# Kernel tuning notes

Hardware: AMD Instinct MI355X
Metric: run time of the kernel (lower is better)

The kernel has to match this reference:

```python
import jax, jax.numpy as jnp
import numpy as np

K = 3          # pred_ks
EMB_SCALE = 1.0


def _unfold(x, k):
    # torch nn.Unfold(kernel=k, padding=(k-1)//2, stride=1), channel-major (C, kh, kw)
    B, C, H, W = x.shape
    p = (k - 1) // 2
    xp = jnp.pad(x, ((0, 0), (0, 0), (p, p), (p, p)))
    pats = jnp.stack([xp[:, :, i:i + H, j:j + W] for i in range(k) for j in range(k)], axis=2)
    return pats.reshape(B, C * k * k, H, W)


def _gs2d_nearest(x, grid):
    # F.grid_sample(mode='nearest', padding_mode='zeros', align_corners=False)
    B, C, H, W = x.shape
    ix = jnp.round((grid[..., 0] + 1.0) * W / 2.0 - 0.5)
    iy = jnp.round((grid[..., 1] + 1.0) * H / 2.0 - 0.5)
    valid = (ix >= 0) & (ix <= W - 1) & (iy >= 0) & (iy <= H - 1)
    ixc = jnp.clip(ix, 0, W - 1).astype(jnp.int32)
    iyc = jnp.clip(iy, 0, H - 1).astype(jnp.int32)

    def samp(img, yy, xx, vv):
        return jnp.where(vv[None], img[:, yy, xx], 0.0)

    return jax.vmap(samp)(x, iyc, ixc, valid)


def _gs3d_trilinear(vol, coords):
    # F.grid_sample 3D, mode='bilinear', padding_mode='zeros', align_corners=False
    # vol [C,D,H,W]; coords [N,3] with (x->W, y->H, z->D)
    C, D, H, W = vol.shape
    x = (coords[:, 0] + 1.0) * W / 2.0 - 0.5
    y = (coords[:, 1] + 1.0) * H / 2.0 - 0.5
    z = (coords[:, 2] + 1.0) * D / 2.0 - 0.5
    x0, y0, z0 = jnp.floor(x), jnp.floor(y), jnp.floor(z)
    vol_f = vol.reshape(C, D * H * W)
    out = jnp.zeros((C, coords.shape[0]), vol.dtype)
    for dz in (0.0, 1.0):
        for dy in (0.0, 1.0):
            for dx in (0.0, 1.0):
                xi, yi, zi = x0 + dx, y0 + dy, z0 + dz
                wgt = (1.0 - jnp.abs(x - xi)) * (1.0 - jnp.abs(y - yi)) * (1.0 - jnp.abs(z - zi))
                valid = (xi >= 0) & (xi <= W - 1) & (yi >= 0) & (yi <= H - 1) & (zi >= 0) & (zi <= D - 1)
                idx = (jnp.clip(zi, 0, D - 1) * (H * W) + jnp.clip(yi, 0, H - 1) * W
                       + jnp.clip(xi, 0, W - 1)).astype(jnp.int32)
                out = out + vol_f[:, idx] * jnp.where(valid, wgt, 0.0)[None]
    return out


def setup_inputs() -> dict:
    key = jax.random.key(0)
    ks = jax.random.split(key, 7)
    B, H, W = 4, 64, 64
    NV, VL, NS = 16, 4, 16
    f = jnp.float32
    grid1 = jax.random.uniform(ks[0], (B, H, W, 2), f, -1.0, 1.0)
    grid2 = jax.random.uniform(ks[1], (B, H, W, 2), f, -1.0, 1.0)
    theta = jax.random.uniform(ks[2], (B,), f, -np.pi, np.pi)
    lgn = jax.random.normal(ks[3], (B, NV * VL, H, W), f)
    coefx = jax.random.uniform(ks[4], (NV, VL, VL, NS), f, -0.1, 0.1)
    coefy = jax.random.uniform(ks[5], (NV, VL, VL, NS), f, -0.1, 0.1)
    coefr = jax.random.uniform(ks[6], (NV, VL, VL, NS), f, -0.1, 0.1)
    return {"grid1": grid1, "grid2": grid2, "theta": theta, "lgn": lgn,
            "coefx": coefx, "coefy": coefy, "coefr": coefr}


def reference(grid1, grid2, theta, lgn, coefx, coefy, coefr):
    B, C, H, W = lgn.shape
    NV, VL, _, NS = coefx.shape
    KS2 = K * K
    # unfold + rearrange to [b, c*ks2, h, w]
    uf_lgn = _unfold(lgn, K)
    uf_g1 = _unfold(jnp.transpose(grid1, (0, 3, 1, 2)), K)
    # nearest-neighbor warps by grid2
    uf_lgn_t = _gs2d_nearest(uf_lgn, grid2)
    uf_g1_t = _gs2d_nearest(uf_g1, grid2)
    g1 = uf_g1_t.reshape(B, 2, KS2, H, W)
    g2 = jnp.transpose(grid2, (0, 3, 1, 2))[:, :, None]          # [b,2,1,h,w]
    d = (g2 - g1) * EMB_SCALE                                    # [b,2,ks2,h,w]
    d = jnp.transpose(d, (0, 2, 3, 4, 1)).reshape(B, KS2 * H * W, 2)
    th = jnp.broadcast_to((theta / np.pi)[:, None, None], (B, KS2 * H * W, 1))
    coords = jnp.concatenate([d, th], axis=-1).reshape(B * KS2 * H * W, 3)
    # separable coefficient volume: x along H-axis, y along D-axis, r along W-axis
    w1 = jnp.einsum('ijkn,iklm->ijlmn', coefx, coefy)            # (nv,vl,vl,D,H)
    coef = jnp.einsum('ijkmn,iklo->ijlmno', w1, coefr)           # (nv,vl,vl,D,H,W)
    vol = coef.reshape(NV * VL * VL, NS, NS, NS)
    samples = _gs3d_trilinear(vol, coords)                       # [nv*vl*vl, b*ks2*h*w]
    coef_ = samples.reshape(NV, VL, VL, B, KS2, H * W)
    coef_ = jnp.transpose(coef_, (3, 5, 4, 0, 1, 2))             # [b,hw,ks2,nv,vl,vl]
    lgn_ = uf_lgn_t.reshape(B, NV, VL, KS2, H * W)
    lgn_ = jnp.transpose(lgn_, (0, 4, 3, 1, 2))                  # [b,hw,ks2,nv,vl]
    pred = jnp.einsum('bsknij,bsknj->bsni', coef_, lgn_)         # matmul + sum over ks2
    return jnp.transpose(pred, (0, 2, 3, 1)).reshape(B, NV * VL, H, W)
```

## Files before the change

kernel.cpp:

```cpp
#include <hip/hip_runtime.h>
#include <hip/hip_fp16.h>
#include <cstdint>

#define BB   4
#define IH   64
#define IW   64
#define HWN  4096
#define NVN  16
#define NSN  16


#define EWS_OFF  (BB*HWN*64*2)
#define CWS_OFF  (EWS_OFF + BB*NVN*NSN*16*2)

struct __align__(16) H2x4 { __half2 h[4]; };
struct __align__(8)  H2x2 { __half2 a, b; };

__global__ __launch_bounds__(256) void prep_kernel(
    const float* __restrict__ lgn, const float* __restrict__ theta,
    const float* __restrict__ coefx, const float* __restrict__ coefy,
    const float* __restrict__ coefr, char* __restrict__ ws)
{
    const int blk = blockIdx.x, t = threadIdx.x;
    if (blk < 512) {
        __shared__ float tile[64][33];
        const int b      = blk >> 7;
        const int hwbase = (blk & 127) << 5;
        const float* src = lgn + (size_t)b * (64 * HWN) + hwbase;
        const int x4 = t & 7;
        const int c0 = t >> 3;
        #pragma unroll
        for (int i = 0; i < 2; ++i) {
            const int c = c0 + i * 32;
            const float4 v = *(const float4*)&src[c * HWN + x4 * 4];
            tile[c][x4 * 4 + 0] = v.x;
            tile[c][x4 * 4 + 1] = v.y;
            tile[c][x4 * 4 + 2] = v.z;
            tile[c][x4 * 4 + 3] = v.w;
        }
        __syncthreads();
        __half2* dst = (__half2*)ws + (size_t)b * (HWN * 32) + (size_t)hwbase * 32;
        const int cp = t & 31, hw0 = t >> 5;
        #pragma unroll
        for (int i = 0; i < 4; ++i) {
            const int hw = hw0 + i * 8;
            dst[hw * 32 + cp] =
                __floats2half2_rn(tile[2 * cp][hw], tile[2 * cp + 1][hw]);
        }
    } else if (blk < 544) {
        const int p  = (blk - 512) * 256 + t;
        const int b  = p >> 11, nv = (p >> 7) & 15, n = (p >> 3) & 15, q = p & 7;
        const float th  = theta[b] * 0.31830988618379067154f;
        const float zf  = (th + 1.0f) * 8.0f - 0.5f;
        const float zfl = floorf(zf);
        const float fz  = zf - zfl;
        const int   m0  = (int)zfl;
        const float wz0 = (m0 >= 0 && m0 <= 15) ? (1.0f - fz) : 0.0f;
        const float wz1 = (m0 + 1 >= 0 && m0 + 1 <= 15) ? fz : 0.0f;
        const int   m0c = min(max(m0, 0), 15), m1c = min(max(m0 + 1, 0), 15);
        float ev[2];
        #pragma unroll
        for (int s = 0; s < 2; ++s) {
            const int idx = 2 * q + s, j = idx >> 2, k2 = idx & 3;
            float e = 0.0f;
            #pragma unroll
            for (int k1 = 0; k1 < 4; ++k1) {
                const float a  = coefx[nv * 256 + (j * 4 + k1) * 16 + n];
                const float bm = wz0 * coefy[nv * 256 + (k1 * 4 + k2) * 16 + m0c]
                               + wz1 * coefy[nv * 256 + (k1 * 4 + k2) * 16 + m1c];
                e += a * bm;
            }
            ev[s] = e;
        }
        ((__half2*)(ws + EWS_OFF))[p] = __floats2half2_rn(ev[0], ev[1]);
    } else {
        const int p = (blk - 544) * 256 + t;
        if (p < 2048) {
            const int nv = p >> 7, o = (p >> 3) & 15, q = p & 7;
            const float c0 = coefr[nv * 256 + (2 * q + 0) * 16 + o];
            const float c1 = coefr[nv * 256 + (2 * q + 1) * 16 + o];
            ((__half2*)(ws + CWS_OFF))[p] = __floats2half2_rn(c0, c1);
        }
    }
}

__global__ __launch_bounds__(256) void seprot_kernel(
    const float* __restrict__ grid1,
    const float* __restrict__ grid2,
    const char*  __restrict__ ws,
    float* __restrict__ out)
{
    __shared__ H2x4 sC[16 * 49];
    __shared__ H2x4 sE[16 * 49];
    __shared__ float sOut[16][17][4];

    const int t   = threadIdx.x;
    const int blk = blockIdx.x;
    const int b      = blk >> 8;
    const int hwbase = (blk & 255) << 4;
    const int pg = t >> 4;
    const int nv = t & 15;
    const int hw = hwbase + pg;

    {
        const H2x4* Cw = (const H2x4*)(ws + CWS_OFF);
        const H2x4* Ew = (const H2x4*)(ws + EWS_OFF) + b * 512;
        #pragma unroll
        for (int k = 0; k < 2; ++k) {
            const int i   = t + k * 256;
            const int wnv = i >> 5, wo = (i >> 1) & 15, wu = i & 1;
            const int du  = wo * 49 + wnv * 3 + wu;
            sC[du] = Cw[i];
            sE[du] = Ew[i];
        }
    }
    __syncthreads();

    const float2 g2  = ((const float2*)grid2)[b * HWN + hw];
    const float  sxf = rintf((g2.x + 1.0f) * (0.5f * IW) - 0.5f);
    const float  syf = rintf((g2.y + 1.0f) * (0.5f * IH) - 0.5f);
    const bool valid = (sxf >= 0.0f) && (sxf <= (float)(IW - 1)) &&
                       (syf >= 0.0f) && (syf <= (float)(IH - 1));

    float acc[4] = {0.0f, 0.0f, 0.0f, 0.0f};

    if (valid) {
        const int sx = (int)sxf, sy = (int)syf;
        const __half2 zero2 = __floats2half2_rn(0.0f, 0.0f);

        #pragma unroll
        for (int tap = 0; tap < 9; ++tap) {
            const int di = tap / 3 - 1, dj = tap % 3 - 1;
            const int ty = sy + di, tx = sx + dj;
            const bool inb = ((unsigned)ty < (unsigned)IH) && ((unsigned)tx < (unsigned)IW);
            const int pix = min(max(ty, 0), IH - 1) * IW + min(max(tx, 0), IW - 1);

            H2x2 lgu = ((const H2x2*)ws)[(b * HWN + pix) * 16 + nv];
            __half2 lg01 = inb ? lgu.a : zero2;
            __half2 lg23 = inb ? lgu.b : zero2;

            const float2 g1 = ((const float2*)grid1)[b * HWN + pix];
            const float dxc = g2.x - g1.x;
            const float dyc = g2.y - g1.y;

            const float xf  = (dxc + 1.0f) * (0.5f * NSN) - 0.5f;
            const float xfl = floorf(xf);
            const float fx  = xf - xfl;
            const int   o0  = (int)xfl;
            const float wx0 = (o0 >= 0 && o0 <= NSN - 1) ? (1.0f - fx) : 0.0f;
            const float wx1 = (o0 + 1 >= 0 && o0 + 1 <= NSN - 1) ? fx : 0.0f;
            const int   o0c = min(max(o0, 0), NSN - 1);
            const int   o1c = min(max(o0 + 1, 0), NSN - 1);

            const float yf  = (dyc + 1.0f) * (0.5f * NSN) - 0.5f;
            const float yfl = floorf(yf);
            const float fy  = yf - yfl;
            const int   n0  = (int)yfl;
            const float wy0 = (n0 >= 0 && n0 <= NSN - 1) ? (1.0f - fy) : 0.0f;
            const float wy1 = (n0 + 1 >= 0 && n0 + 1 <= NSN - 1) ? fy : 0.0f;
            const int   n0c = min(max(n0, 0), NSN - 1);
            const int   n1c = min(max(n0 + 1, 0), NSN - 1);

            const __half2 wx0h = __floats2half2_rn(wx0, wx0);
            const __half2 wx1h = __floats2half2_rn(wx1, wx1);
            const __half2 wy0h = __floats2half2_rn(wy0, wy0);
            const __half2 wy1h = __floats2half2_rn(wy1, wy1);

            const H2x4 c0a = sC[o0c * 49 + nv * 3 + 0];
            const H2x4 c0b = sC[o0c * 49 + nv * 3 + 1];
            const H2x4 c1a = sC[o1c * 49 + nv * 3 + 0];
            const H2x4 c1b = sC[o1c * 49 + nv * 3 + 1];
            __half2 bl[8];
            #pragma unroll
            for (int k = 0; k < 4; ++k) {
                bl[k]     = __hfma2(c0a.h[k], wx0h, __hmul2(c1a.h[k], wx1h));
                bl[4 + k] = __hfma2(c0b.h[k], wx0h, __hmul2(c1b.h[k], wx1h));
            }
            float vf[4];
            #pragma unroll
            for (int k2 = 0; k2 < 4; ++k2) {
                const __half2 sv = __hfma2(bl[2 * k2 + 1], lg23,
                                           __hmul2(bl[2 * k2], lg01));
                vf[k2] = __low2float(sv) + __high2float(sv);
            }
            const __half2 v01 = __floats2half2_rn(vf[0], vf[1]);
            const __half2 v23 = __floats2half2_rn(vf[2], vf[3]);

            const H2x4 e0a = sE[n0c * 49 + nv * 3 + 0];
            const H2x4 e0b = sE[n0c * 49 + nv * 3 + 1];
            const H2x4 e1a = sE[n1c * 49 + nv * 3 + 0];
            const H2x4 e1b = sE[n1c * 49 + nv * 3 + 1];
            __half2 eb[8];
            #pragma unroll
            for (int k = 0; k < 4; ++k) {
                eb[k]     = __hfma2(e0a.h[k], wy0h, __hmul2(e1a.h[k], wy1h));
                eb[4 + k] = __hfma2(e0b.h[k], wy0h, __hmul2(e1b.h[k], wy1h));
            }
            #pragma unroll
            for (int j = 0; j < 4; ++j) {
                const __half2 sa = __hfma2(eb[2 * j + 1], v23,
                                           __hmul2(eb[2 * j], v01));
                acc[j] += __low2float(sa) + __high2float(sa);
            }
        }
    }

    *(float4*)&sOut[pg][nv][0] = make_float4(acc[0], acc[1], acc[2], acc[3]);
    __syncthreads();
    {
        const int nv2 = t >> 4, pg2 = t & 15;
        #pragma unroll
        for (int j = 0; j < 4; ++j)
            out[(b * 64 + nv2 * 4 + j) * HWN + hwbase + pg2] = sOut[pg2][nv2][j];
    }
}

extern "C" void kernel_launch(void* const* d_in, const int* in_sizes, int n_in,
                              void* d_out, int out_size, void* d_ws, size_t ws_size,
                              hipStream_t stream) {
    const float* grid1 = (const float*)d_in[0];
    const float* grid2 = (const float*)d_in[1];
    const float* theta = (const float*)d_in[2];
    const float* lgn   = (const float*)d_in[3];
    const float* coefx = (const float*)d_in[4];
    const float* coefy = (const float*)d_in[5];
    const float* coefr = (const float*)d_in[6];
    float*       outp  = (float*)d_out;
    char*        ws    = (char*)d_ws;

    hipLaunchKernelGGL(prep_kernel, dim3(552), dim3(256), 0, stream,
                       lgn, theta, coefx, coefy, coefr, ws);

    hipLaunchKernelGGL(seprot_kernel, dim3(BB * 256), dim3(256), 0, stream,
                       grid1, grid2, ws, outp);
}
```

Before: 82.61 us.

## Prefetch all tap gathers up front, use fdot2, drop validity branch

```diff
diff --git a/kernel.cpp b/kernel.cpp
--- a/kernel.cpp
+++ b/kernel.cpp
@@ -15,6 +15,14 @@
 
 struct __align__(16) H2x4 { __half2 h[4]; };
 struct __align__(8)  H2x2 { __half2 a, b; };
+
+typedef _Float16 hvec2 __attribute__((ext_vector_type(2)));
+
+static __device__ __forceinline__ float fdot2f(__half2 a, __half2 b, float c) {
+    union { __half2 h; hvec2 v; } ua, ub;
+    ua.h = a; ub.h = b;
+    return __builtin_amdgcn_fdot2(ua.v, ub.v, c, false);
+}
 
 __global__ __launch_bounds__(256) void prep_kernel(
     const float* __restrict__ lgn, const float* __restrict__ theta,
@@ -84,7 +92,7 @@
     }
 }
 
-__global__ __launch_bounds__(256) void seprot_kernel(
+__global__ __launch_bounds__(256, 4) void seprot_kernel(
     const float* __restrict__ grid1,
     const float* __restrict__ grid2,
     const char*  __restrict__ ws,
@@ -121,89 +129,93 @@
     const float  syf = rintf((g2.y + 1.0f) * (0.5f * IH) - 0.5f);
     const bool valid = (sxf >= 0.0f) && (sxf <= (float)(IW - 1)) &&
                        (syf >= 0.0f) && (syf <= (float)(IH - 1));
-
-    float acc[4] = {0.0f, 0.0f, 0.0f, 0.0f};
-
-    if (valid) {
-        const int sx = (int)sxf, sy = (int)syf;
-        const __half2 zero2 = __floats2half2_rn(0.0f, 0.0f);
-
+    const int sx = (int)fminf(fmaxf(sxf, 0.0f), 63.0f);
+    const int sy = (int)fminf(fmaxf(syf, 0.0f), 63.0f);
+
+    H2x2   lgu[9];
+    float2 g1t[9];
+    bool   inb[9];
+    {
+        const H2x2*   lgb = (const H2x2*)ws + (b * HWN) * 16 + nv;
+        const float2* g1b = (const float2*)grid1 + b * HWN;
         #pragma unroll
         for (int tap = 0; tap < 9; ++tap) {
             const int di = tap / 3 - 1, dj = tap % 3 - 1;
             const int ty = sy + di, tx = sx + dj;
-            const bool inb = ((unsigned)ty < (unsigned)IH) && ((unsigned)tx < (unsigned)IW);
+            inb[tap] = ((unsigned)ty < (unsigned)IH) && ((unsigned)tx < (unsigned)IW);
             const int pix = min(max(ty, 0), IH - 1) * IW + min(max(tx, 0), IW - 1);
-
-            H2x2 lgu = ((const H2x2*)ws)[(b * HWN + pix) * 16 + nv];
-            __half2 lg01 = inb ? lgu.a : zero2;
-            __half2 lg23 = inb ? lgu.b : zero2;
-
-            const float2 g1 = ((const float2*)grid1)[b * HWN + pix];
-            const float dxc = g2.x - g1.x;
-            const float dyc = g2.y - g1.y;
-
-            const float xf  = (dxc + 1.0f) * (0.5f * NSN) - 0.5f;
-            const float xfl = floorf(xf);
-            const float fx  = xf - xfl;
-            const int   o0  = (int)xfl;
-            const float wx0 = (o0 >= 0 && o0 <= NSN - 1) ? (1.0f - fx) : 0.0f;
-            const float wx1 = (o0 + 1 >= 0 && o0 + 1 <= NSN - 1) ? fx : 0.0f;
-            const int   o0c = min(max(o0, 0), NSN - 1);
-            const int   o1c = min(max(o0 + 1, 0), NSN - 1);
-
-            const float yf  = (dyc + 1.0f) * (0.5f * NSN) - 0.5f;
-            const float yfl = floorf(yf);
-            const float fy  = yf - yfl;
-            const int   n0  = (int)yfl;
-            const float wy0 = (n0 >= 0 && n0 <= NSN - 1) ? (1.0f - fy) : 0.0f;
-            const float wy1 = (n0 + 1 >= 0 && n0 + 1 <= NSN - 1) ? fy : 0.0f;
-            const int   n0c = min(max(n0, 0), NSN - 1);
-            const int   n1c = min(max(n0 + 1, 0), NSN - 1);
-
-            const __half2 wx0h = __floats2half2_rn(wx0, wx0);
-            const __half2 wx1h = __floats2half2_rn(wx1, wx1);
-            const __half2 wy0h = __floats2half2_rn(wy0, wy0);
-            const __half2 wy1h = __floats2half2_rn(wy1, wy1);
-
-            const H2x4 c0a = sC[o0c * 49 + nv * 3 + 0];
-            const H2x4 c0b = sC[o0c * 49 + nv * 3 + 1];
-            const H2x4 c1a = sC[o1c * 49 + nv * 3 + 0];
-            const H2x4 c1b = sC[o1c * 49 + nv * 3 + 1];
-            __half2 bl[8];
-            #pragma unroll
-            for (int k = 0; k < 4; ++k) {
-                bl[k]     = __hfma2(c0a.h[k], wx0h, __hmul2(c1a.h[k], wx1h));
-                bl[4 + k] = __hfma2(c0b.h[k], wx0h, __hmul2(c1b.h[k], wx1h));
-            }
-            float vf[4];
-            #pragma unroll
-            for (int k2 = 0; k2 < 4; ++k2) {
-                const __half2 sv = __hfma2(bl[2 * k2 + 1], lg23,
-                                           __hmul2(bl[2 * k2], lg01));
-                vf[k2] = __low2float(sv) + __high2float(sv);
-            }
-            const __half2 v01 = __floats2half2_rn(vf[0], vf[1]);
-            const __half2 v23 = __floats2half2_rn(vf[2], vf[3]);
-
-            const H2x4 e0a = sE[n0c * 49 + nv * 3 + 0];
-            const H2x4 e0b = sE[n0c * 49 + nv * 3 + 1];
-            const H2x4 e1a = sE[n1c * 49 + nv * 3 + 0];
-            const H2x4 e1b = sE[n1c * 49 + nv * 3 + 1];
-            __half2 eb[8];
-            #pragma unroll
-            for (int k = 0; k < 4; ++k) {
-                eb[k]     = __hfma2(e0a.h[k], wy0h, __hmul2(e1a.h[k], wy1h));
-                eb[4 + k] = __hfma2(e0b.h[k], wy0h, __hmul2(e1b.h[k], wy1h));
-            }
-            #pragma unroll
-            for (int j = 0; j < 4; ++j) {
-                const __half2 sa = __hfma2(eb[2 * j + 1], v23,
-                                           __hmul2(eb[2 * j], v01));
-                acc[j] += __low2float(sa) + __high2float(sa);
-            }
-        }
-    }
+            lgu[tap] = lgb[pix * 16];
+            g1t[tap] = g1b[pix];
+        }
+    }
+
+    float acc[4] = {0.0f, 0.0f, 0.0f, 0.0f};
+    const __half2 zero2 = __floats2half2_rn(0.0f, 0.0f);
+
+    #pragma unroll
+    for (int tap = 0; tap < 9; ++tap) {
+        const __half2 lg01 = inb[tap] ? lgu[tap].a : zero2;
+        const __half2 lg23 = inb[tap] ? lgu[tap].b : zero2;
+        const float dxc = g2.x - g1t[tap].x;
+        const float dyc = g2.y - g1t[tap].y;
+
+        const float xf  = (dxc + 1.0f) * (0.5f * NSN) - 0.5f;
+        const float xfl = floorf(xf);
+        const float fx  = xf - xfl;
+        const int   o0  = (int)xfl;
+        const float wx0 = (o0 >= 0 && o0 <= NSN - 1) ? (1.0f - fx) : 0.0f;
+        const float wx1 = (o0 + 1 >= 0 && o0 + 1 <= NSN - 1) ? fx : 0.0f;
+        const int   o0c = min(max(o0, 0), NSN - 1);
+        const int   o1c = min(max(o0 + 1, 0), NSN - 1);
+
+        const float yf  = (dyc + 1.0f) * (0.5f * NSN) - 0.5f;
+        const float yfl = floorf(yf);
+        const float fy  = yf - yfl;
+        const int   n0  = (int)yfl;
+        const float wy0 = (n0 >= 0 && n0 <= NSN - 1) ? (1.0f - fy) : 0.0f;
+        const float wy1 = (n0 + 1 >= 0 && n0 + 1 <= NSN - 1) ? fy : 0.0f;
+        const int   n0c = min(max(n0, 0), NSN - 1);
+        const int   n1c = min(max(n0 + 1, 0), NSN - 1);
+
+        const __half2 wx0h = __floats2half2_rn(wx0, wx0);
+        const __half2 wx1h = __floats2half2_rn(wx1, wx1);
+        const __half2 wy0h = __floats2half2_rn(wy0, wy0);
+        const __half2 wy1h = __floats2half2_rn(wy1, wy1);
+
+        const H2x4 c0a = sC[o0c * 49 + nv * 3 + 0];
+        const H2x4 c0b = sC[o0c * 49 + nv * 3 + 1];
+        const H2x4 c1a = sC[o1c * 49 + nv * 3 + 0];
+        const H2x4 c1b = sC[o1c * 49 + nv * 3 + 1];
+        __half2 bl[8];
+        #pragma unroll
+        for (int k = 0; k < 4; ++k) {
+            bl[k]     = __hfma2(c0a.h[k], wx0h, __hmul2(c1a.h[k], wx1h));
+            bl[4 + k] = __hfma2(c0b.h[k], wx0h, __hmul2(c1b.h[k], wx1h));
+        }
+        float vf[4];
+        #pragma unroll
+        for (int k2 = 0; k2 < 4; ++k2)
+            vf[k2] = fdot2f(bl[2 * k2 + 1], lg23, fdot2f(bl[2 * k2], lg01, 0.0f));
+        const __half2 v01 = __floats2half2_rn(vf[0], vf[1]);
+        const __half2 v23 = __floats2half2_rn(vf[2], vf[3]);
+
+        const H2x4 e0a = sE[n0c * 49 + nv * 3 + 0];
+        const H2x4 e0b = sE[n0c * 49 + nv * 3 + 1];
+        const H2x4 e1a = sE[n1c * 49 + nv * 3 + 0];
+        const H2x4 e1b = sE[n1c * 49 + nv * 3 + 1];
+        __half2 eb[8];
+        #pragma unroll
+        for (int k = 0; k < 4; ++k) {
+            eb[k]     = __hfma2(e0a.h[k], wy0h, __hmul2(e1a.h[k], wy1h));
+            eb[4 + k] = __hfma2(e0b.h[k], wy0h, __hmul2(e1b.h[k], wy1h));
+        }
+        #pragma unroll
+        for (int j = 0; j < 4; ++j)
+            acc[j] = fdot2f(eb[2 * j + 1], v23, fdot2f(eb[2 * j], v01, acc[j]));
+    }
+
+    #pragma unroll
+    for (int j = 0; j < 4; ++j) acc[j] = valid ? acc[j] : 0.0f;
 
     *(float4*)&sOut[pg][nv][0] = make_float4(acc[0], acc[1], acc[2], acc[3]);
     __syncthreads();
```

Result: slower. 92.79 us (+12.3%).

## Split the nine stencil taps across two thread halves and reduce with shuffles

Applied to the files above, without the earlier changes.

```diff
diff --git a/kernel.cpp b/kernel.cpp
--- a/kernel.cpp
+++ b/kernel.cpp
@@ -90,16 +90,18 @@
     const char*  __restrict__ ws,
     float* __restrict__ out)
 {
-    __shared__ H2x4 sC[16 * 49];
-    __shared__ H2x4 sE[16 * 49];
-    __shared__ float sOut[16][17][4];
+    __shared__ __align__(16) char smem[2 * 16 * 49 * 16];
+    H2x4* sC = (H2x4*)smem;
+    H2x4* sE = (H2x4*)(smem + 16 * 49 * 16);
+    float (*sOut)[17][4] = (float (*)[17][4])smem;
 
     const int t   = threadIdx.x;
     const int blk = blockIdx.x;
-    const int b      = blk >> 8;
-    const int hwbase = (blk & 255) << 4;
-    const int pg = t >> 4;
+    const int b      = blk >> 9;
+    const int hwbase = (blk & 511) << 3;
     const int nv = t & 15;
+    const int th = (t >> 4) & 1;
+    const int pg = t >> 5;
     const int hw = hwbase + pg;
 
     {
@@ -127,19 +129,24 @@
     if (valid) {
         const int sx = (int)sxf, sy = (int)syf;
         const __half2 zero2 = __floats2half2_rn(0.0f, 0.0f);
-
-        #pragma unroll
-        for (int tap = 0; tap < 9; ++tap) {
-            const int di = tap / 3 - 1, dj = tap % 3 - 1;
+        const H2x2*   lgb = (const H2x2*)ws + (b * HWN) * 16 + nv;
+        const float2* g1b = (const float2*)grid1 + b * HWN;
+
+        #pragma unroll
+        for (int i = 0; i < 5; ++i) {
+            const int tap = th * 5 + i;
+            const int tp  = min(tap, 8);
+            const int di = tp / 3 - 1, dj = tp % 3 - 1;
             const int ty = sy + di, tx = sx + dj;
-            const bool inb = ((unsigned)ty < (unsigned)IH) && ((unsigned)tx < (unsigned)IW);
+            const bool inb = (tap < 9) &&
+                             ((unsigned)ty < (unsigned)IH) && ((unsigned)tx < (unsigned)IW);
             const int pix = min(max(ty, 0), IH - 1) * IW + min(max(tx, 0), IW - 1);
 
-            H2x2 lgu = ((const H2x2*)ws)[(b * HWN + pix) * 16 + nv];
-            __half2 lg01 = inb ? lgu.a : zero2;
-            __half2 lg23 = inb ? lgu.b : zero2;
-
-            const float2 g1 = ((const float2*)grid1)[b * HWN + pix];
+            H2x2 lgu = lgb[pix * 16];
+            const __half2 lg01 = inb ? lgu.a : zero2;
+            const __half2 lg23 = inb ? lgu.b : zero2;
+
+            const float2 g1 = g1b[pix];
             const float dxc = g2.x - g1.x;
             const float dyc = g2.y - g1.y;
 
@@ -205,13 +212,20 @@
         }
     }
 
-    *(float4*)&sOut[pg][nv][0] = make_float4(acc[0], acc[1], acc[2], acc[3]);
+    #pragma unroll
+    for (int j = 0; j < 4; ++j)
+        acc[j] += __shfl_xor(acc[j], 16, 64);
+
+    __syncthreads();
+    if (th == 0)
+        *(float4*)&sOut[pg][nv][0] = make_float4(acc[0], acc[1], acc[2], acc[3]);
     __syncthreads();
     {
-        const int nv2 = t >> 4, pg2 = t & 15;
-        #pragma unroll
-        for (int j = 0; j < 4; ++j)
-            out[(b * 64 + nv2 * 4 + j) * HWN + hwbase + pg2] = sOut[pg2][nv2][j];
+        const int ch = t >> 2;
+        const int p0 = (t & 3) * 2;
+        const int nv2 = ch >> 2, j = ch & 3;
+        float2 v2 = make_float2(sOut[p0][nv2][j], sOut[p0 + 1][nv2][j]);
+        *(float2*)&out[(b * 64 + ch) * HWN + hwbase + p0] = v2;
     }
 }
 
@@ -231,6 +245,6 @@
     hipLaunchKernelGGL(prep_kernel, dim3(552), dim3(256), 0, stream,
                        lgn, theta, coefx, coefy, coefr, ws);
 
-    hipLaunchKernelGGL(seprot_kernel, dim3(BB * 256), dim3(256), 0, stream,
+    hipLaunchKernelGGL(seprot_kernel, dim3(BB * 512), dim3(256), 0, stream,
                        grid1, grid2, ws, outp);
 }
```

New measurement: 83.58 us. About the same (+1.2%).
